# Optimization experiments

Hardware: AMD Instinct MI355X
Metric: run time of the kernel (lower is better)

The kernel has to match this reference:

```python
import jax, jax.numpy as jnp
import numpy as np
import math

DIM = 1536; NH = 12; HD = 128
F, H, W = 6, 30, 30
S = F * H * W
B = 1
K_LEN = 9900  # hardcoded k_lens in the source forward
EPS_NORM = 1e-6


def _rope_tables(max_len=1024, d=HD):
    # Wan rope_params: three tables of widths d-4*(d//6), 2*(d//6), 2*(d//6)
    # -> cos/sin tables of half-widths 22, 21, 21 (concat = d//2 = 64)
    def ang(dd):
        inv = 1.0 / (10000.0 ** (np.arange(0, dd, 2, dtype=np.float64) / dd))
        return np.outer(np.arange(max_len, dtype=np.float64), inv)
    a = np.concatenate([ang(d - 4 * (d // 6)), ang(2 * (d // 6)), ang(2 * (d // 6))], axis=1)
    return np.cos(a).astype(np.float32), np.sin(a).astype(np.float32)


def setup_inputs() -> dict:
    key = jax.random.key(0)
    ks = jax.random.split(key, 5)
    s = 1.0 / math.sqrt(DIM)
    cos, sin = _rope_tables()
    return {
        "x": jax.random.normal(ks[0], (B, S, DIM), jnp.float32),
        "q_w": jax.random.normal(ks[1], (DIM, DIM), jnp.float32) * s,
        "q_b": jnp.zeros((DIM,), jnp.float32),
        "k_w": jax.random.normal(ks[2], (DIM, DIM), jnp.float32) * s,
        "k_b": jnp.zeros((DIM,), jnp.float32),
        "v_w": jax.random.normal(ks[3], (DIM, DIM), jnp.float32) * s,
        "v_b": jnp.zeros((DIM,), jnp.float32),
        "o_w": jax.random.normal(ks[4], (DIM, DIM), jnp.float32) * s,
        "o_b": jnp.zeros((DIM,), jnp.float32),
        "norm_q_w": jnp.ones((DIM,), jnp.float32),
        "norm_k_w": jnp.ones((DIM,), jnp.float32),
        "freqs_cos": jnp.asarray(cos),
        "freqs_sin": jnp.asarray(sin),
        "grid_f": F, "grid_h": H, "grid_w": W,
    }


def rms_norm(x, w):
    # RMSNorm over full model dim, computed in fp32 (as in source)
    xf = x.astype(jnp.float32)
    xn = xf * jax.lax.rsqrt(jnp.mean(xf * xf, axis=-1, keepdims=True) + EPS_NORM)
    return xn.astype(x.dtype) * w


def rope_apply(x, cos, sin, f, h, w):
    # x: [B,S,N,D]; rotate consecutive pairs with 3D-factorized (f,h,w) freqs
    Bb, Ss, Nn, Dd = x.shape
    c = Dd // 2
    sp = [c - 2 * (c // 3), c // 3, c // 3]  # 22, 21, 21

    def grid(tab):
        tf = tab[:, :sp[0]]
        th = tab[:, sp[0]:sp[0] + sp[1]]
        tw = tab[:, sp[0] + sp[1]:]
        g = jnp.concatenate([
            jnp.broadcast_to(tf[:f, None, None, :], (f, h, w, sp[0])),
            jnp.broadcast_to(th[None, :h, None, :], (f, h, w, sp[1])),
            jnp.broadcast_to(tw[None, None, :w, :], (f, h, w, sp[2])),
        ], axis=-1)
        return g.reshape(f * h * w, 1, c)  # [S,1,c] (broadcast over heads)

    gc, gs = grid(cos), grid(sin)
    xp = x.astype(jnp.float32).reshape(Bb, Ss, Nn, c, 2)
    xr, xi = xp[..., 0], xp[..., 1]
    orr = xr * gc - xi * gs
    oii = xr * gs + xi * gc
    return jnp.stack([orr, oii], axis=-1).reshape(Bb, Ss, Nn, Dd).astype(x.dtype)


def attention(q, k, v, k_len):
    # full attention (window_size=(-1,-1)) with keys masked beyond k_len
    scale = 1.0 / math.sqrt(q.shape[-1])
    att = jnp.einsum('bqnd,bknd->bnqk', q, k) * scale
    valid = jnp.arange(k.shape[1]) < k_len
    att = jnp.where(valid[None, None, None, :], att, jnp.finfo(att.dtype).min)
    p = jax.nn.softmax(att, axis=-1)
    return jnp.einsum('bnqk,bknd->bqnd', p, v)


def reference(x, q_w, q_b, k_w, k_b, v_w, v_b, o_w, o_b, norm_q_w, norm_k_w, freqs_cos, freqs_sin, grid_f, grid_h, grid_w):
    Bb, Ss, _ = x.shape
    q = rms_norm(x @ q_w.T + q_b, norm_q_w).reshape(Bb, Ss, NH, HD)
    k = rms_norm(x @ k_w.T + k_b, norm_k_w).reshape(Bb, Ss, NH, HD)
    v = (x @ v_w.T + v_b).reshape(Bb, Ss, NH, HD)
    q = rope_apply(q, freqs_cos, freqs_sin, grid_f, grid_h, grid_w)
    k = rope_apply(k, freqs_cos, freqs_sin, grid_f, grid_h, grid_w)
    o = attention(q, k, v, K_LEN).reshape(Bb, Ss, NH * HD)
    return o @ o_w.T + o_b
```

## Files before the change

kernel.cpp:

```cpp
#include <hip/hip_runtime.h>

#define DIM 1536
#define NH 12
#define HD 128
#define S_LEN 5400
#define SPAD 5440
#define MPAD 5504
#define NQKV 4608
#define EPS_NORM 1e-6f

typedef __bf16 bf16_t;
typedef __bf16 bf16x8 __attribute__((ext_vector_type(8)));
typedef __bf16 bf16x4 __attribute__((ext_vector_type(4)));
typedef float  f32x4  __attribute__((ext_vector_type(4)));

#define GLOAD_LDS16(gp, lp) __builtin_amdgcn_global_load_lds( \
    (__attribute__((address_space(1))) void*)(void*)(gp),     \
    (__attribute__((address_space(3))) void*)(lp), 16, 0, 0)


__global__ __launch_bounds__(256) void cvt_x_kernel(const float* __restrict__ x,
                                                    bf16_t* __restrict__ xb) {
  size_t base = ((size_t)blockIdx.x * 256 + threadIdx.x) * 4;
  if (base >= (size_t)MPAD * DIM) return;
  size_t row = base / DIM;
  float4 v = make_float4(0.f, 0.f, 0.f, 0.f);
  if (row < S_LEN) v = *(const float4*)&x[base];
  bf16x4 o; o[0] = (__bf16)v.x; o[1] = (__bf16)v.y; o[2] = (__bf16)v.z; o[3] = (__bf16)v.w;
  *(bf16x4*)&xb[base] = o;
}

__global__ __launch_bounds__(256) void cvt_wqkv_kernel(const float* __restrict__ qw,
                                                       const float* __restrict__ kw,
                                                       const float* __restrict__ vw,
                                                       bf16_t* __restrict__ wb) {
  size_t base = ((size_t)blockIdx.x * 256 + threadIdx.x) * 4;
  if (base >= (size_t)NQKV * DIM) return;
  int row = (int)(base / DIM);
  int col = (int)(base - (size_t)row * DIM);
  const float* src; int rr = row;
  if (rr >= 3072)      { src = vw; rr -= 3072; }
  else if (rr >= 1536) { src = kw; rr -= 1536; }
  else                 { src = qw; }
  float4 v = *(const float4*)&src[(size_t)rr * DIM + col];
  bf16x4 o; o[0] = (__bf16)v.x; o[1] = (__bf16)v.y; o[2] = (__bf16)v.z; o[3] = (__bf16)v.w;
  *(bf16x4*)&wb[base] = o;
}

__global__ __launch_bounds__(256) void cvt_wo_kernel(const float* __restrict__ w,
                                                     bf16_t* __restrict__ wb) {
  size_t base = ((size_t)blockIdx.x * 256 + threadIdx.x) * 4;
  if (base >= (size_t)DIM * DIM) return;
  float4 v = *(const float4*)&w[base];
  bf16x4 o; o[0] = (__bf16)v.x; o[1] = (__bf16)v.y; o[2] = (__bf16)v.z; o[3] = (__bf16)v.w;
  *(bf16x4*)&wb[base] = o;
}


template<bool OUT_BF16>
__global__ __launch_bounds__(256) void gemm_bt_kernel(
    const bf16_t* __restrict__ A, const bf16_t* __restrict__ B, void* __restrict__ C,
    const float* __restrict__ bias0, const float* __restrict__ bias1,
    const float* __restrict__ bias2, int M, int N, int K, int Mvalid) {
  __shared__ bf16_t As[128 * 32];
  __shared__ bf16_t Bs[128 * 32];
  int tid = threadIdx.x;
  int lane = tid & 63, wave = tid >> 6, quad = lane >> 4, l16 = lane & 15;
  int m0 = blockIdx.y * 128, n0 = blockIdx.x * 128;
  int wm = (wave >> 1) * 64, wn = (wave & 1) * 64;
  const bf16_t* Ab = A + (size_t)m0 * K;
  const bf16_t* Bb = B + (size_t)n0 * K;
  f32x4 acc[4][4] = {};
  for (int kt = 0; kt < K; kt += 32) {
    __syncthreads();
#pragma unroll
    for (int i = 0; i < 2; i++) {
      int eo = (i * 256 + tid) * 8;
      int row = eo >> 5, col = eo & 31;
      GLOAD_LDS16(Ab + (size_t)row * K + kt + col, &As[eo]);
      GLOAD_LDS16(Bb + (size_t)row * K + kt + col, &Bs[eo]);
    }
    __syncthreads();
    bf16x8 af[4], bfr[4];
#pragma unroll
    for (int i = 0; i < 4; i++)
      af[i] = *(const bf16x8*)&As[(wm + i * 16 + l16) * 32 + quad * 8];
#pragma unroll
    for (int j = 0; j < 4; j++)
      bfr[j] = *(const bf16x8*)&Bs[(wn + j * 16 + l16) * 32 + quad * 8];
#pragma unroll
    for (int i = 0; i < 4; i++)
#pragma unroll
      for (int j = 0; j < 4; j++)
        acc[i][j] = __builtin_amdgcn_mfma_f32_16x16x32_bf16(af[i], bfr[j], acc[i][j], 0, 0, 0);
  }
#pragma unroll
  for (int j = 0; j < 4; j++) {
    int n = n0 + wn + j * 16 + l16;
    float bias = (n < 1536) ? bias0[n] : (n < 3072) ? bias1[n - 1536] : bias2[n - 3072];
#pragma unroll
    for (int i = 0; i < 4; i++) {
#pragma unroll
      for (int r = 0; r < 4; r++) {
        int m = m0 + wm + i * 16 + quad * 4 + r;
        float v = acc[i][j][r] + bias;
        if (OUT_BF16) {
          ((bf16_t*)C)[(size_t)m * N + n] = (__bf16)v;
        } else {
          if (m < Mvalid) ((float*)C)[(size_t)m * N + n] = v;
        }
      }
    }
  }
}


__global__ __launch_bounds__(256) void rope_qk_kernel(
    const bf16_t* __restrict__ qkv, const float* __restrict__ nqw,
    const float* __restrict__ nkw, const float* __restrict__ fcos,
    const float* __restrict__ fsin, bf16_t* __restrict__ qout,
    bf16_t* __restrict__ kout) {
  int s = blockIdx.x;
  int tid = threadIdx.x;
  bool valid = s < S_LEN;
  int f = s / 900, hh = (s / 30) % 30, ww = s % 30;
  __shared__ float red[4];
  for (int which = 0; which < 2; which++) {
    const bf16_t* src = qkv + (size_t)s * NQKV + which * DIM;
    const float* nw = which ? nkw : nqw;
    bf16_t* dst = (which ? kout : qout) + (size_t)s * DIM;
    float osc = which ? 1.0f : 0.08838834764831845f;
    float v[6]; float ss = 0.f;
#pragma unroll
    for (int i = 0; i < 6; i++) {
      v[i] = valid ? (float)src[tid * 6 + i] : 0.f;
      ss += v[i] * v[i];
    }
#pragma unroll
    for (int off = 32; off >= 1; off >>= 1) ss += __shfl_down(ss, off);
    if ((tid & 63) == 0) red[tid >> 6] = ss;
    __syncthreads();
    float tot = red[0] + red[1] + red[2] + red[3];
    float rn = rsqrtf(tot * (1.f / DIM) + EPS_NORM);
    __syncthreads();
#pragma unroll
    for (int i = 0; i < 3; i++) {
      int e0 = tid * 6 + 2 * i;
      int p = e0 >> 1;
      int cc = p & 63;
      int pos = (cc < 22) ? f : (cc < 43) ? hh : ww;
      float c = fcos[pos * 64 + cc], sn = fsin[pos * 64 + cc];
      float xr = v[2 * i] * rn * nw[e0];
      float xi = v[2 * i + 1] * rn * nw[e0 + 1];
      dst[e0]     = (__bf16)((xr * c - xi * sn) * osc);
      dst[e0 + 1] = (__bf16)((xr * sn + xi * c) * osc);
    }
  }
}


__global__ __launch_bounds__(256) void v_transpose_kernel(const bf16_t* __restrict__ qkv,
                                                          bf16_t* __restrict__ vt) {
  __shared__ bf16_t tile[64][136];
  int h = blockIdx.y, s0 = blockIdx.x * 64, tid = threadIdx.x;
#pragma unroll
  for (int it = 0; it < 4; it++) {
    int eo = (it * 256 + tid) * 8;
    int row = eo >> 7, col = eo & 127;
    int s = s0 + row;
    bf16x8 val = {};
    if (s < S_LEN) val = *(const bf16x8*)&qkv[(size_t)s * NQKV + 3072 + h * HD + col];
    *(bf16x8*)&tile[row][col] = val;
  }
  __syncthreads();
  int d = tid & 127, j0 = (tid >> 7) * 32;
  bf16x8 outv[4];
#pragma unroll
  for (int b = 0; b < 4; b++)
#pragma unroll
    for (int j = 0; j < 8; j++) outv[b][j] = tile[j0 + b * 8 + j][d];
  size_t base = ((size_t)h * HD + d) * SPAD + s0 + j0;
#pragma unroll
  for (int b = 0; b < 4; b++) *(bf16x8*)&vt[base + b * 8] = outv[b];
}


__global__ __launch_bounds__(256, 3) void flash_attn_kernel(
    const bf16_t* __restrict__ q, const bf16_t* __restrict__ k,
    const bf16_t* __restrict__ vt, bf16_t* __restrict__ o) {
  __shared__ bf16_t smem[16384];
  bf16_t* Ks = smem;
  bf16_t* Vs = smem + 8192;
  int h = blockIdx.y;
  int s0 = blockIdx.x * 128;
  int tid = threadIdx.x, w = tid >> 6, lane = tid & 63;
  int quad = lane >> 4, l16 = lane & 15;

  bf16x8 bq[2][4];
#pragma unroll
  for (int g = 0; g < 2; g++)
#pragma unroll
    for (int ks = 0; ks < 4; ks++) {
      int qrow = s0 + w * 32 + g * 16 + l16;
      bq[g][ks] = *(const bf16x8*)&q[(size_t)qrow * DIM + h * HD + ks * 32 + quad * 8];
    }

  float m_i[2] = {-1e30f, -1e30f}, l_i[2] = {0.f, 0.f};
  f32x4 oacc[2][8] = {};
  int sA = (quad & 1) * 32 + l16;
  int sB = sA + 16;
  bool selhi = quad >= 2;

  for (int kt = 0; kt < SPAD; kt += 64) {
    __syncthreads();
#pragma unroll
    for (int it = 0; it < 4; it++) {
      int slot = it * 256 + tid;
      int row = slot >> 4, pc = slot & 15;
      int c = (pc & 8) | ((pc & 7) ^ (row & 7));
      GLOAD_LDS16(k + (size_t)(kt + row) * DIM + h * HD + c * 8, &Ks[slot * 8]);
    }
#pragma unroll
    for (int it = 0; it < 4; it++) {
      int slot = it * 256 + tid;
      int d = slot >> 3, pc = slot & 7;
      int c = pc ^ (d & 7);
      GLOAD_LDS16(vt + ((size_t)h * HD + d) * SPAD + kt + c * 8, &Vs[slot * 8]);
    }
    __syncthreads();

    f32x4 sacc[2][4] = {};
#pragma unroll
    for (int ns = 0; ns < 4; ns++) {
      bf16x8 ak[4];
#pragma unroll
      for (int ks = 0; ks < 4; ks++) {
        int row = ns * 16 + l16;
        int ch = ks * 4 + quad;
        int pc = (ch & 8) | ((ch & 7) ^ (l16 & 7));
        ak[ks] = *(const bf16x8*)&Ks[row * 128 + pc * 8];
      }
#pragma unroll
      for (int g = 0; g < 2; g++)
#pragma unroll
        for (int ks = 0; ks < 4; ks++)
          sacc[g][ns] = __builtin_amdgcn_mfma_f32_16x16x32_bf16(ak[ks], bq[g][ks], sacc[g][ns], 0, 0, 0);
    }

    bool full = (kt + 64 <= S_LEN);
    unsigned int pkl[2][4], pkh[2][4];
#pragma unroll
    for (int g = 0; g < 2; g++) {
      if (!full) {
#pragma unroll
        for (int ns = 0; ns < 4; ns++)
#pragma unroll
          for (int r = 0; r < 4; r++)
            if (kt + ns * 16 + quad * 4 + r >= S_LEN) sacc[g][ns][r] = -1e30f;
      }
      float mx = -1e30f;
#pragma unroll
      for (int ns = 0; ns < 4; ns++)
#pragma unroll
        for (int r = 0; r < 4; r++) mx = fmaxf(mx, sacc[g][ns][r]);
      mx = fmaxf(mx, __shfl_xor(mx, 16));
      mx = fmaxf(mx, __shfl_xor(mx, 32));
      float mn = fmaxf(m_i[g], mx);
      float al = __expf(m_i[g] - mn);
      m_i[g] = mn;
      float rs = 0.f;
#pragma unroll
      for (int ns = 0; ns < 4; ns++) {
        bf16x4 pk;
#pragma unroll
        for (int r = 0; r < 4; r++) {
          float p = __expf(sacc[g][ns][r] - mn);
          rs += p;
          pk[r] = (__bf16)p;
        }
        union { bf16x4 v; unsigned int u[2]; } cv; cv.v = pk;
        pkl[g][ns] = cv.u[0]; pkh[g][ns] = cv.u[1];
      }
      rs += __shfl_xor(rs, 16);
      rs += __shfl_xor(rs, 32);
      l_i[g] = l_i[g] * al + rs;
#pragma unroll
      for (int dt = 0; dt < 8; dt++) oacc[g][dt] *= al;
    }

#pragma unroll
    for (int ks = 0; ks < 2; ks++) {
      bf16x8 bp[2];
#pragma unroll
      for (int g = 0; g < 2; g++) {
        int b0 = __shfl((int)pkl[g][2 * ks], sA);
        int b1 = __shfl((int)pkh[g][2 * ks], sA);
        int b2 = __shfl((int)pkl[g][2 * ks], sB);
        int b3 = __shfl((int)pkh[g][2 * ks], sB);
        int c0 = __shfl((int)pkl[g][2 * ks + 1], sA);
        int c1 = __shfl((int)pkh[g][2 * ks + 1], sA);
        int c2 = __shfl((int)pkl[g][2 * ks + 1], sB);
        int c3 = __shfl((int)pkh[g][2 * ks + 1], sB);
        union { unsigned int u[4]; bf16x8 v; } cv;
        cv.u[0] = selhi ? (unsigned)c0 : (unsigned)b0;
        cv.u[1] = selhi ? (unsigned)c1 : (unsigned)b1;
        cv.u[2] = selhi ? (unsigned)c2 : (unsigned)b2;
        cv.u[3] = selhi ? (unsigned)c3 : (unsigned)b3;
        bp[g] = cv.v;
      }
#pragma unroll
      for (int dt = 0; dt < 8; dt++) {
        int ch = ks * 4 + quad;
        int pc = ch ^ (l16 & 7);
        bf16x8 av = *(const bf16x8*)&Vs[(dt * 16 + l16) * 64 + pc * 8];
#pragma unroll
        for (int g = 0; g < 2; g++)
          oacc[g][dt] = __builtin_amdgcn_mfma_f32_16x16x32_bf16(av, bp[g], oacc[g][dt], 0, 0, 0);
      }
    }
  }

  __syncthreads();
  bf16_t* Ot = smem;
#pragma unroll
  for (int g = 0; g < 2; g++) {
    float inv = 1.f / l_i[g];
#pragma unroll
    for (int dt = 0; dt < 8; dt++) {
      bf16x4 v;
#pragma unroll
      for (int r = 0; r < 4; r++) v[r] = (__bf16)(oacc[g][dt][r] * inv);
      int qrow = w * 32 + g * 16 + l16;
      int c = dt * 2 + (quad >> 1);
      int pc = (c & 8) | ((c & 7) ^ (l16 & 7));
      *(bf16x4*)&Ot[qrow * 128 + pc * 8 + (quad & 1) * 4] = v;
    }
  }
  __syncthreads();
#pragma unroll
  for (int i = 0; i < 8; i++) {
    int q_ = i * 16 + (tid >> 4);
    int cc = tid & 15;
    int pc = (cc & 8) | ((cc & 7) ^ (q_ & 7));
    bf16x8 val = *(const bf16x8*)&Ot[q_ * 128 + pc * 8];
    int s = s0 + q_;
    if (s < S_LEN) *(bf16x8*)&o[(size_t)s * DIM + h * HD + cc * 8] = val;
  }
}


extern "C" void kernel_launch(void* const* d_in, const int* in_sizes, int n_in,
                              void* d_out, int out_size, void* d_ws, size_t ws_size,
                              hipStream_t stream) {
  const float* x    = (const float*)d_in[0];
  const float* q_w  = (const float*)d_in[1];
  const float* q_b  = (const float*)d_in[2];
  const float* k_w  = (const float*)d_in[3];
  const float* k_b  = (const float*)d_in[4];
  const float* v_w  = (const float*)d_in[5];
  const float* v_b  = (const float*)d_in[6];
  const float* o_w  = (const float*)d_in[7];
  const float* o_b  = (const float*)d_in[8];
  const float* nqw  = (const float*)d_in[9];
  const float* nkw  = (const float*)d_in[10];
  const float* fcos = (const float*)d_in[11];
  const float* fsin = (const float*)d_in[12];

  char* ws = (char*)d_ws;
  bf16_t* xb   = (bf16_t*)(ws + 0);
  bf16_t* wqkv = (bf16_t*)(ws + 16908288);
  bf16_t* wob  = (bf16_t*)(ws + 31064064);
  bf16_t* qkv  = (bf16_t*)(ws + 35782656);
  bf16_t* qb   = (bf16_t*)(ws + 86507520);
  bf16_t* kb   = (bf16_t*)(ws + 103415808);
  bf16_t* vtb  = (bf16_t*)(ws + 0);
  bf16_t* aob  = (bf16_t*)(ws + 35782656);

  cvt_x_kernel<<<(MPAD * DIM / 4 + 255) / 256, 256, 0, stream>>>(x, xb);
  cvt_wqkv_kernel<<<(NQKV * DIM / 4 + 255) / 256, 256, 0, stream>>>(q_w, k_w, v_w, wqkv);
  cvt_wo_kernel<<<(DIM * DIM / 4 + 255) / 256, 256, 0, stream>>>(o_w, wob);

  gemm_bt_kernel<true><<<dim3(NQKV / 128, MPAD / 128), 256, 0, stream>>>(
      xb, wqkv, qkv, q_b, k_b, v_b, MPAD, NQKV, DIM, MPAD);

  rope_qk_kernel<<<MPAD, 256, 0, stream>>>(qkv, nqw, nkw, fcos, fsin, qb, kb);
  v_transpose_kernel<<<dim3(SPAD / 64, NH), 256, 0, stream>>>(qkv, vtb);

  flash_attn_kernel<<<dim3(MPAD / 128, NH), 256, 0, stream>>>(qb, kb, vtb, aob);

  gemm_bt_kernel<false><<<dim3(DIM / 128, MPAD / 128), 256, 0, stream>>>(
      aob, wob, d_out, o_b, o_b, o_b, MPAD, DIM, DIM, S_LEN);
}
```

Measured before the change: 742.8 us.

## Halve flash-attention query tile to 64 rows and raise occupancy to four blocks

Each flash-attention block now handles 64 query rows instead of 128, so each wave keeps a single 16-row query group rather than two. The grid doubles to about 1032 blocks and launch bounds allow four blocks per CU, fixing the poor CU fill of the old 516-block grid. In exchange, K/V tiles are reused across half as many queries, doubling K/V traffic from L2. Each wave also has less independent MFMA work to hide latency, and a small tail of blocks may spill past one full wave of residency.

After: 750.6 us. About the same (+1.1%).

```diff
diff --git a/kernel.cpp b/kernel.cpp
--- a/kernel.cpp
+++ b/kernel.cpp
@@ -185,28 +185,26 @@
 }
 
 
-__global__ __launch_bounds__(256, 3) void flash_attn_kernel(
+__global__ __launch_bounds__(256, 4) void flash_attn_kernel(
     const bf16_t* __restrict__ q, const bf16_t* __restrict__ k,
     const bf16_t* __restrict__ vt, bf16_t* __restrict__ o) {
   __shared__ bf16_t smem[16384];
   bf16_t* Ks = smem;
   bf16_t* Vs = smem + 8192;
   int h = blockIdx.y;
-  int s0 = blockIdx.x * 128;
+  int s0 = blockIdx.x * 64;
   int tid = threadIdx.x, w = tid >> 6, lane = tid & 63;
   int quad = lane >> 4, l16 = lane & 15;
 
-  bf16x8 bq[2][4];
-#pragma unroll
-  for (int g = 0; g < 2; g++)
-#pragma unroll
-    for (int ks = 0; ks < 4; ks++) {
-      int qrow = s0 + w * 32 + g * 16 + l16;
-      bq[g][ks] = *(const bf16x8*)&q[(size_t)qrow * DIM + h * HD + ks * 32 + quad * 8];
-    }
-
-  float m_i[2] = {-1e30f, -1e30f}, l_i[2] = {0.f, 0.f};
-  f32x4 oacc[2][8] = {};
+  bf16x8 bq[4];
+#pragma unroll
+  for (int ks = 0; ks < 4; ks++) {
+    int qrow = s0 + w * 16 + l16;
+    bq[ks] = *(const bf16x8*)&q[(size_t)qrow * DIM + h * HD + ks * 32 + quad * 8];
+  }
+
+  float m_i = -1e30f, l_i = 0.f;
+  f32x4 oacc[8] = {};
   int sA = (quad & 1) * 32 + l16;
   int sB = sA + 16;
   bool selhi = quad >= 2;
@@ -229,7 +227,7 @@
     }
     __syncthreads();
 
-    f32x4 sacc[2][4] = {};
+    f32x4 sacc[4] = {};
 #pragma unroll
     for (int ns = 0; ns < 4; ns++) {
       bf16x8 ak[4];
@@ -241,96 +239,84 @@
         ak[ks] = *(const bf16x8*)&Ks[row * 128 + pc * 8];
       }
 #pragma unroll
-      for (int g = 0; g < 2; g++)
-#pragma unroll
-        for (int ks = 0; ks < 4; ks++)
-          sacc[g][ns] = __builtin_amdgcn_mfma_f32_16x16x32_bf16(ak[ks], bq[g][ks], sacc[g][ns], 0, 0, 0);
+      for (int ks = 0; ks < 4; ks++)
+        sacc[ns] = __builtin_amdgcn_mfma_f32_16x16x32_bf16(ak[ks], bq[ks], sacc[ns], 0, 0, 0);
     }
 
     bool full = (kt + 64 <= S_LEN);
-    unsigned int pkl[2][4], pkh[2][4];
-#pragma unroll
-    for (int g = 0; g < 2; g++) {
-      if (!full) {
-#pragma unroll
-        for (int ns = 0; ns < 4; ns++)
-#pragma unroll
-          for (int r = 0; r < 4; r++)
-            if (kt + ns * 16 + quad * 4 + r >= S_LEN) sacc[g][ns][r] = -1e30f;
+    unsigned int pkl[4], pkh[4];
+    if (!full) {
+#pragma unroll
+      for (int ns = 0; ns < 4; ns++)
+#pragma unroll
+        for (int r = 0; r < 4; r++)
+          if (kt + ns * 16 + quad * 4 + r >= S_LEN) sacc[ns][r] = -1e30f;
+    }
+    float mx = -1e30f;
+#pragma unroll
+    for (int ns = 0; ns < 4; ns++)
+#pragma unroll
+      for (int r = 0; r < 4; r++) mx = fmaxf(mx, sacc[ns][r]);
+    mx = fmaxf(mx, __shfl_xor(mx, 16));
+    mx = fmaxf(mx, __shfl_xor(mx, 32));
+    float mn = fmaxf(m_i, mx);
+    float al = __expf(m_i - mn);
+    m_i = mn;
+    float rs = 0.f;
+#pragma unroll
+    for (int ns = 0; ns < 4; ns++) {
+      bf16x4 pk;
+#pragma unroll
+      for (int r = 0; r < 4; r++) {
+        float p = __expf(sacc[ns][r] - mn);
+        rs += p;
+        pk[r] = (__bf16)p;
       }
-      float mx = -1e30f;
-#pragma unroll
-      for (int ns = 0; ns < 4; ns++)
-#pragma unroll
-        for (int r = 0; r < 4; r++) mx = fmaxf(mx, sacc[g][ns][r]);
-      mx = fmaxf(mx, __shfl_xor(mx, 16));
-      mx = fmaxf(mx, __shfl_xor(mx, 32));
-      float mn = fmaxf(m_i[g], mx);
-      float al = __expf(m_i[g] - mn);
-      m_i[g] = mn;
-      float rs = 0.f;
-#pragma unroll
-      for (int ns = 0; ns < 4; ns++) {
-        bf16x4 pk;
-#pragma unroll
-        for (int r = 0; r < 4; r++) {
-          float p = __expf(sacc[g][ns][r] - mn);
-          rs += p;
-          pk[r] = (__bf16)p;
-        }
-        union { bf16x4 v; unsigned int u[2]; } cv; cv.v = pk;
-        pkl[g][ns] = cv.u[0]; pkh[g][ns] = cv.u[1];
-      }
-      rs += __shfl_xor(rs, 16);
-      rs += __shfl_xor(rs, 32);
-      l_i[g] = l_i[g] * al + rs;
-#pragma unroll
-      for (int dt = 0; dt < 8; dt++) oacc[g][dt] *= al;
-    }
+      union { bf16x4 v; unsigned int u[2]; } cv; cv.v = pk;
+      pkl[ns] = cv.u[0]; pkh[ns] = cv.u[1];
+    }
+    rs += __shfl_xor(rs, 16);
+    rs += __shfl_xor(rs, 32);
+    l_i = l_i * al + rs;
+#pragma unroll
+    for (int dt = 0; dt < 8; dt++) oacc[dt] *= al;
 
 #pragma unroll
     for (int ks = 0; ks < 2; ks++) {
-      bf16x8 bp[2];
-#pragma unroll
-      for (int g = 0; g < 2; g++) {
-        int b0 = __shfl((int)pkl[g][2 * ks], sA);
-        int b1 = __shfl((int)pkh[g][2 * ks], sA);
-        int b2 = __shfl((int)pkl[g][2 * ks], sB);
-        int b3 = __shfl((int)pkh[g][2 * ks], sB);
-        int c0 = __shfl((int)pkl[g][2 * ks + 1], sA);
-        int c1 = __shfl((int)pkh[g][2 * ks + 1], sA);
-        int c2 = __shfl((int)pkl[g][2 * ks + 1], sB);
-        int c3 = __shfl((int)pkh[g][2 * ks + 1], sB);
-        union { unsigned int u[4]; bf16x8 v; } cv;
-        cv.u[0] = selhi ? (unsigned)c0 : (unsigned)b0;
-        cv.u[1] = selhi ? (unsigned)c1 : (unsigned)b1;
-        cv.u[2] = selhi ? (unsigned)c2 : (unsigned)b2;
-        cv.u[3] = selhi ? (unsigned)c3 : (unsigned)b3;
-        bp[g] = cv.v;
-      }
+      int b0 = __shfl((int)pkl[2 * ks], sA);
+      int b1 = __shfl((int)pkh[2 * ks], sA);
+      int b2 = __shfl((int)pkl[2 * ks], sB);
+      int b3 = __shfl((int)pkh[2 * ks], sB);
+      int c0 = __shfl((int)pkl[2 * ks + 1], sA);
+      int c1 = __shfl((int)pkh[2 * ks + 1], sA);
+      int c2 = __shfl((int)pkl[2 * ks + 1], sB);
+      int c3 = __shfl((int)pkh[2 * ks + 1], sB);
+      union { unsigned int u[4]; bf16x8 v; } cv;
+      cv.u[0] = selhi ? (unsigned)c0 : (unsigned)b0;
+      cv.u[1] = selhi ? (unsigned)c1 : (unsigned)b1;
+      cv.u[2] = selhi ? (unsigned)c2 : (unsigned)b2;
+      cv.u[3] = selhi ? (unsigned)c3 : (unsigned)b3;
+      bf16x8 bp = cv.v;
 #pragma unroll
       for (int dt = 0; dt < 8; dt++) {
         int ch = ks * 4 + quad;
         int pc = ch ^ (l16 & 7);
         bf16x8 av = *(const bf16x8*)&Vs[(dt * 16 + l16) * 64 + pc * 8];
-#pragma unroll
-        for (int g = 0; g < 2; g++)
-          oacc[g][dt] = __builtin_amdgcn_mfma_f32_16x16x32_bf16(av, bp[g], oacc[g][dt], 0, 0, 0);
+        oacc[dt] = __builtin_amdgcn_mfma_f32_16x16x32_bf16(av, bp, oacc[dt], 0, 0, 0);
       }
     }
   }
 
   __syncthreads();
   bf16_t* Ot = smem;
-#pragma unroll
-  for (int g = 0; g < 2; g++) {
-    float inv = 1.f / l_i[g];
+  {
+    float inv = 1.f / l_i;
 #pragma unroll
     for (int dt = 0; dt < 8; dt++) {
       bf16x4 v;
 #pragma unroll
-      for (int r = 0; r < 4; r++) v[r] = (__bf16)(oacc[g][dt][r] * inv);
-      int qrow = w * 32 + g * 16 + l16;
+      for (int r = 0; r < 4; r++) v[r] = (__bf16)(oacc[dt][r] * inv);
+      int qrow = w * 16 + l16;
       int c = dt * 2 + (quad >> 1);
       int pc = (c & 8) | ((c & 7) ^ (l16 & 7));
       *(bf16x4*)&Ot[qrow * 128 + pc * 8 + (quad & 1) * 4] = v;
@@ -338,7 +324,7 @@
   }
   __syncthreads();
 #pragma unroll
-  for (int i = 0; i < 8; i++) {
+  for (int i = 0; i < 4; i++) {
     int q_ = i * 16 + (tid >> 4);
     int cc = tid & 15;
     int pc = (cc & 8) | ((cc & 7) ^ (q_ & 7));
@@ -386,7 +372,7 @@
   rope_qk_kernel<<<MPAD, 256, 0, stream>>>(qkv, nqw, nkw, fcos, fsin, qb, kb);
   v_transpose_kernel<<<dim3(SPAD / 64, NH), 256, 0, stream>>>(qkv, vtb);
 
-  flash_attn_kernel<<<dim3(MPAD / 128, NH), 256, 0, stream>>>(qb, kb, vtb, aob);
+  flash_attn_kernel<<<dim3(MPAD / 64, NH), 256, 0, stream>>>(qb, kb, vtb, aob);
 
   gemm_bt_kernel<false><<<dim3(DIM / 128, MPAD / 128), 256, 0, stream>>>(
       aob, wob, d_out, o_b, o_b, o_b, MPAD, DIM, DIM, S_LEN);
```
